# Performance work log

Measured on AMD Instinct MI355X. Metric: run time of the kernel, lower is better.

## Reference

```python
import jax, jax.numpy as jnp
import numpy as np

B, H, W, C = 32, 32, 32, 256


def setup_inputs() -> dict:
    key = jax.random.key(0)
    k1, k2 = jax.random.split(key)
    feats1 = jax.random.normal(k1, (B, H, W, C), dtype=jnp.float32)
    feats2 = jax.random.normal(k2, (B, H, W, C), dtype=jnp.float32)
    return {"feats1": feats1, "feats2": feats2}


def reference(feats1, feats2):
    # Training path of LocalFeatureLoss (trainflag=True)
    b, h, w, c = feats1.shape
    l = h * w
    q = feats1.reshape(b, l, c)  # queries: (B, l, C)
    p = feats2.reshape(b, l, c)  # preds:   (B, l, C)
    # M[b, a, j] = <p[b,a], q[b,j]>  == fm2 @ fm1.T per batch
    M = jnp.einsum('bac,bjc->baj', p, q)  # (B, l_pred, l_query)
    max1 = jnp.argmax(M, axis=1)  # (B, l_q): best pred index for each query token
    max2 = jnp.argmax(M, axis=2)  # (B, l_p): best query index for each pred token
    # mutual nearest-neighbor check: m[b, j] = max2[b, max1[b, j]]
    m = jnp.take_along_axis(max2, max1, axis=1)  # (B, l_q)
    valid = jnp.arange(l)[None, :] == m          # (B, l_q) bool
    # gather matched pred descriptors and compute per-pair similarity
    matched_p = jnp.take_along_axis(p, max1[..., None], axis=1)  # (B, l_q, C)
    sims = jnp.sum(q * matched_p, axis=-1)                        # (B, l_q)
    cnt = jnp.sum(valid, axis=1).astype(sims.dtype)               # (B,)
    # mean over mutual NN pairs (torch mean over idx1)
    similarity = jnp.sum(jnp.where(valid, sims, 0.0), axis=1) / jnp.maximum(cnt, 1.0)
    return similarity
```

## Files before the change

### kernel.cpp

```cpp
#include <hip/hip_runtime.h>
#include <hip/hip_bf16.h>

#define BATCH 32
#define L 1024
#define CD 256
#define TM 64
#define TN 64
#define NTB 8
#define KC 128
#define RT_PER_B 16
#define SP_LD (CD + 8)
#define SQ_LD (KC + 8)

typedef __bf16 bf16x8 __attribute__((ext_vector_type(8)));
typedef __bf16 bf16x4 __attribute__((ext_vector_type(4)));
typedef float  f32x4  __attribute__((ext_vector_type(4)));

__device__ __forceinline__ unsigned int enc_f32(float f) {
    unsigned int u = __float_as_uint(f);
    return ((int)u < 0) ? ~u : (u | 0x80000000u);
}
__device__ __forceinline__ float dec_f32(unsigned int u) {
    u = (u & 0x80000000u) ? (u & 0x7FFFFFFFu) : ~u;
    return __uint_as_float(u);
}
__device__ __forceinline__ unsigned long long pmax(unsigned long long a, unsigned long long b) {
    return a > b ? a : b;
}
__device__ __forceinline__ bf16x8 cvt8(float4 v0, float4 v1) {
    bf16x8 o;
    o[0] = (__bf16)v0.x; o[1] = (__bf16)v0.y; o[2] = (__bf16)v0.z; o[3] = (__bf16)v0.w;
    o[4] = (__bf16)v1.x; o[5] = (__bf16)v1.y; o[6] = (__bf16)v1.z; o[7] = (__bf16)v1.w;
    return o;
}

__global__ __launch_bounds__(256) void mm_argmax_kernel(
    const float* __restrict__ qg,
    const float* __restrict__ pg,
    unsigned long long* __restrict__ colpart,
    unsigned long long* __restrict__ rowpart)
{
    __shared__ __bf16 sP[TM][SP_LD];
    __shared__ __bf16 sQ[TN][SQ_LD];
    __shared__ unsigned long long sCol[TN];
    __shared__ unsigned long long sRowW[2][TM];

    const int tid = threadIdx.x;
    const int bid = blockIdx.x;
    const int b    = bid & 31;
    const int rth  = bid >> 5;
    const int rt   = rth >> 1;
    const int h    = rth & 1;
    const int row0 = rt * TM;
    const int nt0  = h * NTB;

    const int lane = tid & 63;
    const int w    = tid >> 6;
    const int wm   = w >> 1;
    const int wn   = w & 1;
    const int quad = lane >> 4;
    const int l16  = lane & 15;

    const float* pB = pg + ((size_t)b * L + row0) * CD;
    const float* qB = qg + (size_t)b * L * CD;

    const int sr = tid >> 2;
    const int sc = tid & 3;
    {
        const float4* src = (const float4*)(pB + sr * CD);
        #pragma unroll
        for (int i = 0; i < 8; ++i) {
            const int s0 = 2 * sc + 8 * i;
            *(bf16x8*)&sP[sr][s0 * 4] = cvt8(src[s0], src[s0 + 1]);
        }
    }

    float4 pf[8];
    {
        const float4* src = (const float4*)(qB + (size_t)(nt0 * TN + sr) * CD);
        #pragma unroll
        for (int i = 0; i < 4; ++i) {
            const int s0 = 2 * sc + 8 * i;
            pf[2 * i]     = src[s0];
            pf[2 * i + 1] = src[s0 + 1];
        }
    }

    unsigned long long rowbest[2][4];
    #pragma unroll
    for (int tm = 0; tm < 2; ++tm)
        #pragma unroll
        for (int r = 0; r < 4; ++r) rowbest[tm][r] = 0ull;
    unsigned long long pend[2] = {0ull, 0ull};

    for (int t = 0; t < NTB; ++t) {
        const int nt = nt0 + t;
        f32x4 acc[2][2];
        #pragma unroll
        for (int tm = 0; tm < 2; ++tm)
            #pragma unroll
            for (int tn = 0; tn < 2; ++tn) acc[tm][tn] = (f32x4){0.f, 0.f, 0.f, 0.f};

        for (int kc = 0; kc < 2; ++kc) {
            if (t || kc) __syncthreads();
            if (kc == 0 && t > 0 && wm == 1 && quad == 0) {
                #pragma unroll
                for (int tn = 0; tn < 2; ++tn) {
                    const int c = wn * 32 + tn * 16 + l16;
                    colpart[((size_t)b * RT_PER_B + rt) * L + (nt - 1) * TN + c] =
                        pmax(pend[tn], sCol[c]);
                }
            }
            #pragma unroll
            for (int i = 0; i < 4; ++i) {
                const int s0 = 2 * sc + 8 * i;
                *(bf16x8*)&sQ[sr][s0 * 4] = cvt8(pf[2 * i], pf[2 * i + 1]);
            }
            if (!(t == NTB - 1 && kc == 1)) {
                const int nnt = (kc == 0) ? nt : nt + 1;
                const int nkc = kc ^ 1;
                const float4* src = (const float4*)(qB + (size_t)(nnt * TN + sr) * CD + nkc * KC);
                #pragma unroll
                for (int i = 0; i < 4; ++i) {
                    const int s0 = 2 * sc + 8 * i;
                    pf[2 * i]     = src[s0];
                    pf[2 * i + 1] = src[s0 + 1];
                }
            }
            __syncthreads();
            #pragma unroll
            for (int kk = 0; kk < 4; ++kk) {
                const int ka = kc * KC + kk * 32 + quad * 8;
                const int kb = kk * 32 + quad * 8;
                bf16x8 a0 = *(const bf16x8*)&sP[wm * 32 +      l16][ka];
                bf16x8 a1 = *(const bf16x8*)&sP[wm * 32 + 16 + l16][ka];
                bf16x8 b0 = *(const bf16x8*)&sQ[wn * 32 +      l16][kb];
                bf16x8 b1 = *(const bf16x8*)&sQ[wn * 32 + 16 + l16][kb];
                acc[0][0] = __builtin_amdgcn_mfma_f32_16x16x32_bf16(a0, b0, acc[0][0], 0, 0, 0);
                acc[0][1] = __builtin_amdgcn_mfma_f32_16x16x32_bf16(a0, b1, acc[0][1], 0, 0, 0);
                acc[1][0] = __builtin_amdgcn_mfma_f32_16x16x32_bf16(a1, b0, acc[1][0], 0, 0, 0);
                acc[1][1] = __builtin_amdgcn_mfma_f32_16x16x32_bf16(a1, b1, acc[1][1], 0, 0, 0);
            }
        }

        #pragma unroll
        for (int tn = 0; tn < 2; ++tn) {
            const unsigned int jcol = (unsigned int)(nt * TN + wn * 32 + tn * 16 + l16);
            const unsigned long long jpk = (unsigned long long)(unsigned int)(~jcol);
            unsigned long long cbest = 0ull;
            #pragma unroll
            for (int tm = 0; tm < 2; ++tm) {
                #pragma unroll
                for (int r = 0; r < 4; ++r) {
                    const unsigned int e = enc_f32(acc[tm][tn][r]);
                    const unsigned int aidx =
                        (unsigned int)(row0 + wm * 32 + tm * 16 + quad * 4 + r);
                    cbest = pmax(cbest, ((unsigned long long)e << 32) | (unsigned int)(~aidx));
                    rowbest[tm][r] = pmax(rowbest[tm][r], ((unsigned long long)e << 32) | jpk);
                }
            }
            cbest = pmax(cbest, __shfl_xor(cbest, 16));
            cbest = pmax(cbest, __shfl_xor(cbest, 32));
            if (quad == 0) {
                const int c = wn * 32 + tn * 16 + l16;
                if (wm == 0) sCol[c] = cbest;
                else         pend[tn] = cbest;
            }
        }
    }

    __syncthreads();
    if (wm == 1 && quad == 0) {
        #pragma unroll
        for (int tn = 0; tn < 2; ++tn) {
            const int c = wn * 32 + tn * 16 + l16;
            colpart[((size_t)b * RT_PER_B + rt) * L + (nt0 + NTB - 1) * TN + c] =
                pmax(pend[tn], sCol[c]);
        }
    }

    #pragma unroll
    for (int tm = 0; tm < 2; ++tm) {
        #pragma unroll
        for (int r = 0; r < 4; ++r) {
            unsigned long long pk = rowbest[tm][r];
            pk = pmax(pk, __shfl_xor(pk, 1));
            pk = pmax(pk, __shfl_xor(pk, 2));
            pk = pmax(pk, __shfl_xor(pk, 4));
            pk = pmax(pk, __shfl_xor(pk, 8));
            rowbest[tm][r] = pk;
        }
    }
    if (l16 == 0) {
        #pragma unroll
        for (int tm = 0; tm < 2; ++tm)
            #pragma unroll
            for (int r = 0; r < 4; ++r)
                sRowW[wn][wm * 32 + tm * 16 + quad * 4 + r] = rowbest[tm][r];
    }
    __syncthreads();
    if (w == 0) {
        unsigned long long m = pmax(sRowW[0][lane], sRowW[1][lane]);
        rowpart[(((size_t)b * RT_PER_B + rt) * 2 + h) * TM + lane] = m;
    }
}

__global__ __launch_bounds__(256) void finalize_kernel(
    const unsigned long long* __restrict__ colpart,
    const unsigned long long* __restrict__ rowpart,
    float* __restrict__ out)
{
    __shared__ int sMax2[L];
    __shared__ float sSum[4];
    __shared__ int sCnt[4];
    const int b = blockIdx.x;
    const int tid = threadIdx.x;

    for (int i = tid; i < L; i += 256) {
        const int rt = i >> 6, a = i & 63;
        const size_t base = (((size_t)b * RT_PER_B + rt) * 2) * TM + a;
        unsigned long long m = pmax(rowpart[base], rowpart[base + TM]);
        sMax2[i] = (int)(~(unsigned int)m);
    }
    __syncthreads();

    float sum = 0.f;
    int cnt = 0;
    #pragma unroll
    for (int i = 0; i < 4; ++i) {
        const int j = tid + i * 256;
        unsigned long long best = 0ull;
        #pragma unroll
        for (int rt = 0; rt < RT_PER_B; ++rt)
            best = pmax(best, colpart[((size_t)b * RT_PER_B + rt) * L + j]);
        const int a = (int)(~(unsigned int)best) & (L - 1);
        const float val = dec_f32((unsigned int)(best >> 32));
        if (sMax2[a] == j) { sum += val; ++cnt; }
    }
    #pragma unroll
    for (int o = 32; o >= 1; o >>= 1) {
        sum += __shfl_down(sum, o);
        cnt += __shfl_down(cnt, o);
    }
    if ((tid & 63) == 0) { sSum[tid >> 6] = sum; sCnt[tid >> 6] = cnt; }
    __syncthreads();
    if (tid == 0) {
        float S = sSum[0] + sSum[1] + sSum[2] + sSum[3];
        int   C = sCnt[0] + sCnt[1] + sCnt[2] + sCnt[3];
        out[b] = S / fmaxf((float)C, 1.0f);
    }
}

extern "C" void kernel_launch(void* const* d_in, const int* in_sizes, int n_in,
                              void* d_out, int out_size, void* d_ws, size_t ws_size,
                              hipStream_t stream) {
    const float* q = (const float*)d_in[0];
    const float* p = (const float*)d_in[1];
    float* out = (float*)d_out;

    unsigned long long* colpart = (unsigned long long*)d_ws;
    unsigned long long* rowpart =
        (unsigned long long*)((char*)d_ws + (size_t)BATCH * RT_PER_B * L * sizeof(unsigned long long));

    mm_argmax_kernel<<<BATCH * RT_PER_B * 2, 256, 0, stream>>>(q, p, colpart, rowpart);
    finalize_kernel<<<BATCH, 256, 0, stream>>>(colpart, rowpart, out);
}
```

Baseline: 137.5 us.

## Keep P operand tile in registers instead of LDS; coalesce Q staging loads

Each wave now loads its 32 rows of P directly from global memory into registers as bf16 MFMA fragments, once per block, and the shared-memory P tile is removed. This cuts LDS footprint and per-iteration LDS reads. The Q staging pattern is changed so 16 threads cover one row chunk, which makes global loads more contiguous. Launch bounds now request 3 blocks per SM. The cost is 64 extra VGPRs per thread for the A fragments, which may cause spills under the tighter register cap, and the initial P loads are strided per lane.

```diff
diff --git a/kernel.cpp b/kernel.cpp
--- a/kernel.cpp
+++ b/kernel.cpp
@@ -9,11 +9,9 @@
 #define NTB 8
 #define KC 128
 #define RT_PER_B 16
-#define SP_LD (CD + 8)
 #define SQ_LD (KC + 8)
 
 typedef __bf16 bf16x8 __attribute__((ext_vector_type(8)));
-typedef __bf16 bf16x4 __attribute__((ext_vector_type(4)));
 typedef float  f32x4  __attribute__((ext_vector_type(4)));
 
 __device__ __forceinline__ unsigned int enc_f32(float f) {
@@ -34,13 +32,12 @@
     return o;
 }
 
-__global__ __launch_bounds__(256) void mm_argmax_kernel(
+__global__ __launch_bounds__(256, 3) void mm_argmax_kernel(
     const float* __restrict__ qg,
     const float* __restrict__ pg,
     unsigned long long* __restrict__ colpart,
     unsigned long long* __restrict__ rowpart)
 {
-    __shared__ __bf16 sP[TM][SP_LD];
     __shared__ __bf16 sQ[TN][SQ_LD];
     __shared__ unsigned long long sCol[TN];
     __shared__ unsigned long long sRowW[2][TM];
@@ -61,28 +58,33 @@
     const int quad = lane >> 4;
     const int l16  = lane & 15;
 
-    const float* pB = pg + ((size_t)b * L + row0) * CD;
     const float* qB = qg + (size_t)b * L * CD;
 
-    const int sr = tid >> 2;
-    const int sc = tid & 3;
+    bf16x8 af[2][8];
     {
-        const float4* src = (const float4*)(pB + sr * CD);
-        #pragma unroll
-        for (int i = 0; i < 8; ++i) {
-            const int s0 = 2 * sc + 8 * i;
-            *(bf16x8*)&sP[sr][s0 * 4] = cvt8(src[s0], src[s0 + 1]);
-        }
-    }
+        const float* pA = pg + ((size_t)b * L + row0 + wm * 32) * CD + quad * 8;
+        #pragma unroll
+        for (int tm = 0; tm < 2; ++tm) {
+            const float* prow = pA + (tm * 16 + l16) * CD;
+            #pragma unroll
+            for (int kp = 0; kp < 8; ++kp) {
+                float4 v0 = *(const float4*)(prow + kp * 32);
+                float4 v1 = *(const float4*)(prow + kp * 32 + 4);
+                af[tm][kp] = cvt8(v0, v1);
+            }
+        }
+    }
+
+    const int srow = tid >> 4;
+    const int schk = tid & 15;
 
     float4 pf[8];
     {
-        const float4* src = (const float4*)(qB + (size_t)(nt0 * TN + sr) * CD);
-        #pragma unroll
-        for (int i = 0; i < 4; ++i) {
-            const int s0 = 2 * sc + 8 * i;
-            pf[2 * i]     = src[s0];
-            pf[2 * i + 1] = src[s0 + 1];
+        #pragma unroll
+        for (int j = 0; j < 4; ++j) {
+            const float* src = qB + (size_t)(nt0 * TN + j * 16 + srow) * CD + schk * 8;
+            pf[2 * j]     = *(const float4*)src;
+            pf[2 * j + 1] = *(const float4*)(src + 4);
         }
     }
 
@@ -112,34 +114,30 @@
                 }
             }
             #pragma unroll
-            for (int i = 0; i < 4; ++i) {
-                const int s0 = 2 * sc + 8 * i;
-                *(bf16x8*)&sQ[sr][s0 * 4] = cvt8(pf[2 * i], pf[2 * i + 1]);
-            }
+            for (int j = 0; j < 4; ++j)
+                *(bf16x8*)&sQ[j * 16 + srow][schk * 8] = cvt8(pf[2 * j], pf[2 * j + 1]);
             if (!(t == NTB - 1 && kc == 1)) {
                 const int nnt = (kc == 0) ? nt : nt + 1;
                 const int nkc = kc ^ 1;
-                const float4* src = (const float4*)(qB + (size_t)(nnt * TN + sr) * CD + nkc * KC);
                 #pragma unroll
-                for (int i = 0; i < 4; ++i) {
-                    const int s0 = 2 * sc + 8 * i;
-                    pf[2 * i]     = src[s0];
-                    pf[2 * i + 1] = src[s0 + 1];
+                for (int j = 0; j < 4; ++j) {
+                    const float* src =
+                        qB + (size_t)(nnt * TN + j * 16 + srow) * CD + nkc * KC + schk * 8;
+                    pf[2 * j]     = *(const float4*)src;
+                    pf[2 * j + 1] = *(const float4*)(src + 4);
                 }
             }
             __syncthreads();
             #pragma unroll
             for (int kk = 0; kk < 4; ++kk) {
-                const int ka = kc * KC + kk * 32 + quad * 8;
+                const int kp = kc * 4 + kk;
                 const int kb = kk * 32 + quad * 8;
-                bf16x8 a0 = *(const bf16x8*)&sP[wm * 32 +      l16][ka];
-                bf16x8 a1 = *(const bf16x8*)&sP[wm * 32 + 16 + l16][ka];
                 bf16x8 b0 = *(const bf16x8*)&sQ[wn * 32 +      l16][kb];
                 bf16x8 b1 = *(const bf16x8*)&sQ[wn * 32 + 16 + l16][kb];
-                acc[0][0] = __builtin_amdgcn_mfma_f32_16x16x32_bf16(a0, b0, acc[0][0], 0, 0, 0);
-                acc[0][1] = __builtin_amdgcn_mfma_f32_16x16x32_bf16(a0, b1, acc[0][1], 0, 0, 0);
-                acc[1][0] = __builtin_amdgcn_mfma_f32_16x16x32_bf16(a1, b0, acc[1][0], 0, 0, 0);
-                acc[1][1] = __builtin_amdgcn_mfma_f32_16x16x32_bf16(a1, b1, acc[1][1], 0, 0, 0);
+                acc[0][0] = __builtin_amdgcn_mfma_f32_16x16x32_bf16(af[0][kp], b0, acc[0][0], 0, 0, 0);
+                acc[0][1] = __builtin_amdgcn_mfma_f32_16x16x32_bf16(af[0][kp], b1, acc[0][1], 0, 0, 0);
+                acc[1][0] = __builtin_amdgcn_mfma_f32_16x16x32_bf16(af[1][kp], b0, acc[1][0], 0, 0, 0);
+                acc[1][1] = __builtin_amdgcn_mfma_f32_16x16x32_bf16(af[1][kp], b1, acc[1][1], 0, 0, 0);
             }
         }
 
```

Result: slower. 208.1 us (+51.3%).
